# Kernel optimization log

Hardware: AMD Instinct MI355X
Metric: run time of the kernel (lower is better)

The kernel has to match this reference:

```python
import jax, jax.numpy as jnp
import numpy as np

N_STEPS = 7
N_TERMS = 4


def _sobel_kernel2d():
    dx = jnp.array([[-1.0, 0.0, 1.0], [-2.0, 0.0, 2.0], [-1.0, 0.0, 1.0]], dtype=jnp.float32)
    dy = jnp.array([[-1.0, -2.0, -1.0], [0.0, 0.0, 0.0], [1.0, 2.0, 1.0]], dtype=jnp.float32)
    return 0.125 * jnp.stack([dy, dx, dy, dx], 0)[:, None]  # [4,1,3,3]


def _grid_sample_bilinear(src, sx, sy):
    # src: [N,C,H,W]; sx,sy: [N,H,W] pixel coords (align_corners=False, zeros padding)
    N, C, H, W = src.shape
    x0 = jnp.floor(sx)
    y0 = jnp.floor(sy)
    wx = (sx - x0)[:, None]  # [N,1,H,W]
    wy = (sy - y0)[:, None]
    x0i = x0.astype(jnp.int32)
    y0i = y0.astype(jnp.int32)

    def gather(yi, xi):
        valid = ((xi >= 0) & (xi < W) & (yi >= 0) & (yi < H))
        xc = jnp.clip(xi, 0, W - 1)
        yc = jnp.clip(yi, 0, H - 1)
        v = jax.vmap(lambda im, y, x: im[:, y, x])(src, yc, xc)  # [N,C,H,W]
        return v * valid[:, None].astype(src.dtype)

    v00 = gather(y0i, x0i)
    v01 = gather(y0i, x0i + 1)
    v10 = gather(y0i + 1, x0i)
    v11 = gather(y0i + 1, x0i + 1)
    return (v00 * (1 - wx) * (1 - wy) + v01 * wx * (1 - wy)
            + v10 * (1 - wx) * wy + v11 * wx * wy)


def _transform(src, disp, gy, gx, H, W):
    # new pixel locations; torch normalizes with (size-1) but samples with
    # align_corners=False, net mapping: p -> p*S/(S-1) - 0.5
    py = gy + disp[:, 0]
    px = gx + disp[:, 1]
    sy = py * (H / (H - 1)) - 0.5
    sx = px * (W / (W - 1)) - 0.5
    return _grid_sample_bilinear(src, sx, sy)


def _jacobian2d(vel):
    # replicate-pad then depthwise sobel conv -> [N,2,2,H,W]
    N, _, H, W = vel.shape
    padded = jnp.pad(vel, ((0, 0), (0, 0), (1, 1), (1, 1)), mode='edge')
    jac = jax.lax.conv_general_dilated(
        padded, _sobel_kernel2d(), window_strides=(1, 1), padding='VALID',
        feature_group_count=2, dimension_numbers=('NCHW', 'OIHW', 'NCHW'))
    return jac.reshape(N, 2, 2, H, W)


def _logdet1p(jac, eps):
    # -sum_n (-eps)^n tr(J^n)/n over the 2x2 dims, per pixel -> [N,H,W]
    ld = jnp.zeros(jac.shape[:1] + jac.shape[-2:], dtype=jac.dtype)
    xn = jac
    for n in range(1, N_TERMS + 1):
        if n > 1:
            xn = jnp.einsum('nikhw,nkjhw->nijhw', xn, jac)
        tr = xn[:, 0, 0] + xn[:, 1, 1]
        ld = ld - ((-eps) ** n) * tr / n
    return ld


def _integrate(vel, logdet_jac):
    N, _, H, W = vel.shape
    gy, gx = jnp.meshgrid(jnp.arange(H, dtype=vel.dtype),
                          jnp.arange(W, dtype=vel.dtype), indexing='ij')
    eps = 2.0 ** (-N_STEPS)
    disp = eps * vel
    if logdet_jac:
        ldjac = _logdet1p(_jacobian2d(vel), eps)[:, None]  # [N,1,H,W]
    else:
        ldjac = None
    for _ in range(N_STEPS):
        disp = disp + _transform(disp, disp, gy, gx, H, W)
        if logdet_jac:
            ldjac = ldjac + _transform(ldjac, disp, gy, gx, H, W)
    return disp, ldjac


def setup_inputs() -> dict:
    key = jax.random.key(0)
    vel = jax.random.normal(key, (16, 2, 512, 512), dtype=jnp.float32)
    return {"vel": vel, "logdet_jac": 1}


def reference(vel, logdet_jac):
    return _integrate(vel, bool(logdet_jac))
```

## Files before the change

kernel.cpp:

```cpp
#include <hip/hip_runtime.h>


#define NB 16
#define HH 512
#define WW 512
#define HW (HH * WW)
#define TOT (NB * HW)
#define EPS 0.0078125f
#define DISP_ELEMS (NB * 2 * HW)
#define SC (512.0f / 511.0f)

typedef _Float16 f16;
typedef _Float16 f16x4 __attribute__((ext_vector_type(4)));

struct SampC {
    int yc0, xc0, yc1, xc1;
    float w00, w01, w10, w11;
};

__device__ __forceinline__ SampC make_sampc(float sy, float sx) {
    float fy = floorf(sy), fx = floorf(sx);
    float wy = sy - fy, wx = sx - fx;
    int y0 = (int)fy, x0 = (int)fx;
    int y1 = y0 + 1, x1 = x0 + 1;
    bool xv0 = (unsigned)x0 < (unsigned)WW;
    bool xv1 = (unsigned)x1 < (unsigned)WW;
    bool yv0 = (unsigned)y0 < (unsigned)HH;
    bool yv1 = (unsigned)y1 < (unsigned)HH;
    SampC s;
    s.xc0 = min(max(x0, 0), WW - 1); s.xc1 = min(max(x1, 0), WW - 1);
    s.yc0 = min(max(y0, 0), HH - 1); s.yc1 = min(max(y1, 0), HH - 1);
    float omwx = 1.0f - wx, omwy = 1.0f - wy;
    s.w00 = (xv0 && yv0) ? omwx * omwy : 0.0f;
    s.w01 = (xv1 && yv0) ? wx * omwy   : 0.0f;
    s.w10 = (xv0 && yv1) ? omwx * wy   : 0.0f;
    s.w11 = (xv1 && yv1) ? wx * wy     : 0.0f;
    return s;
}

__device__ __forceinline__ f16x4 step_rec(f16x4 rv, f16x4 g00, f16x4 g01,
                                          f16x4 g10, f16x4 g11, const SampC& s) {
    float d0 = (float)rv.x, d1 = (float)rv.y, l = (float)rv.z;
    float nd0 = d0 + s.w00 * (float)g00.x + s.w01 * (float)g01.x
                   + s.w10 * (float)g10.x + s.w11 * (float)g11.x;
    float nd1 = d1 + s.w00 * (float)g00.y + s.w01 * (float)g01.y
                   + s.w10 * (float)g10.y + s.w11 * (float)g11.y;
    float nl  = l  + s.w00 * (float)g00.z + s.w01 * (float)g01.z
                   + s.w10 * (float)g10.z + s.w11 * (float)g11.z;
    f16x4 w; w.x = (f16)nd0; w.y = (f16)nd1; w.z = (f16)nl; w.w = (f16)0.0f;
    return w;
}

__device__ __forceinline__ float rnd16(float v) { return (float)(f16)v; }

__device__ __forceinline__ void tile_map(int& img, int& ty0, int& tx0) {
    int bidx = blockIdx.x;
    int xcd = bidx & 7, sub = bidx >> 3;
    img = 2 * xcd + (sub >= 256 ? 1 : 0);
    int tile = sub & 255;
    tx0 = (tile & 15) << 5;
    ty0 = (tile >> 4) << 5;
}

__device__ __forceinline__ int remap_idx() {
    int bid = blockIdx.x;
    int task = ((bid & 7) << 11) | (bid >> 3);
    return task * 256 + threadIdx.x;
}

__global__ void __launch_bounds__(256) init_fused(const float* __restrict__ vel,
                                                  f16x4* __restrict__ rdst) {
    int idx = remap_idx();
    int n = idx >> 18;
    int rem = idx & (HW - 1);
    int y = rem >> 9, x = rem & (WW - 1);

    const float* v0 = vel + (size_t)n * 2 * HW;
    const float* v1 = v0 + HW;

    int ym = max(y - 1, 0), yp = min(y + 1, HH - 1);
    int xm = max(x - 1, 0), xp = min(x + 1, WW - 1);
    int r0 = ym * WW, r1 = y * WW, r2 = yp * WW;

    float A00 = v0[r0 + xm], A01 = v0[r0 + x], A02 = v0[r0 + xp];
    float A10 = v0[r1 + xm], A11 = v0[r1 + x], A12 = v0[r1 + xp];
    float A20 = v0[r2 + xm], A21 = v0[r2 + x], A22 = v0[r2 + xp];
    float B00 = v1[r0 + xm], B01 = v1[r0 + x], B02 = v1[r0 + xp];
    float B10 = v1[r1 + xm], B11 = v1[r1 + x], B12 = v1[r1 + xp];
    float B20 = v1[r2 + xm], B21 = v1[r2 + x], B22 = v1[r2 + xp];

    float a = 0.125f * ((A20 + 2.0f * A21 + A22) - (A00 + 2.0f * A01 + A02));
    float b = 0.125f * ((A02 + 2.0f * A12 + A22) - (A00 + 2.0f * A10 + A20));
    float c = 0.125f * ((B20 + 2.0f * B21 + B22) - (B00 + 2.0f * B01 + B02));
    float d = 0.125f * ((B02 + 2.0f * B12 + B22) - (B00 + 2.0f * B10 + B20));

    float xa = a, xb = b, xc = c, xd = d;
    float ld = EPS * (xa + xd);
    float na = xa * a + xb * c, nb = xa * b + xb * d;
    float nc = xc * a + xd * c, nd = xc * b + xd * d;
    xa = na; xb = nb; xc = nc; xd = nd;
    ld -= (EPS * EPS) * (xa + xd) * 0.5f;
    na = xa * a + xb * c; nb = xa * b + xb * d;
    nc = xc * a + xd * c; nd = xc * b + xd * d;
    xa = na; xb = nb; xc = nc; xd = nd;
    ld += (EPS * EPS * EPS) * (xa + xd) * (1.0f / 3.0f);
    na = xa * a + xb * c;
    nd = xc * b + xd * d;
    ld -= (EPS * EPS * EPS * EPS) * (na + nd) * 0.25f;

    float d0 = rnd16(EPS * A11);
    float d1 = rnd16(EPS * B11);

    float sy = fmaf((float)y + d0, SC, -0.5f);
    float sx = fmaf((float)x + d1, SC, -0.5f);
    SampC s = make_sampc(sy, sx);

    bool rlo = (sy < (float)y);
    bool clo = (sx < (float)x);

    float Ar0c0 = rlo ? A00 : A10, Ar0c1 = rlo ? A01 : A11, Ar0c2 = rlo ? A02 : A12;
    float Ar1c0 = rlo ? A10 : A20, Ar1c1 = rlo ? A11 : A21, Ar1c2 = rlo ? A12 : A22;
    float Br0c0 = rlo ? B00 : B10, Br0c1 = rlo ? B01 : B11, Br0c2 = rlo ? B02 : B12;
    float Br1c0 = rlo ? B10 : B20, Br1c1 = rlo ? B11 : B21, Br1c2 = rlo ? B12 : B22;

    float g00x = rnd16(EPS * (clo ? Ar0c0 : Ar0c1));
    float g01x = rnd16(EPS * (clo ? Ar0c1 : Ar0c2));
    float g10x = rnd16(EPS * (clo ? Ar1c0 : Ar1c1));
    float g11x = rnd16(EPS * (clo ? Ar1c1 : Ar1c2));
    float g00y = rnd16(EPS * (clo ? Br0c0 : Br0c1));
    float g01y = rnd16(EPS * (clo ? Br0c1 : Br0c2));
    float g10y = rnd16(EPS * (clo ? Br1c0 : Br1c1));
    float g11y = rnd16(EPS * (clo ? Br1c1 : Br1c2));

    float nd0 = d0 + s.w00 * g00x + s.w01 * g01x + s.w10 * g10x + s.w11 * g11x;
    float nd1 = d1 + s.w00 * g00y + s.w01 * g01y + s.w10 * g10y + s.w11 * g11y;

    f16x4 rec;
    rec.x = (f16)nd0; rec.y = (f16)nd1; rec.z = (f16)ld; rec.w = (f16)0.0f;
    rdst[(size_t)n * HW + rem] = rec;
}

template <int R1, int R2, int R3>
__global__ void __launch_bounds__(256, 4) step_triple(const f16x4* __restrict__ rsrc,
                                                      f16x4* __restrict__ rdst) {
    constexpr int M2d = 32 + 2 * R3;
    constexpr int M1d = 32 + 2 * (R2 + R3);
    constexpr int Ed  = 32 + 2 * (R1 + R2 + R3);
    __shared__ __align__(16) f16x4 IN[Ed][Ed + 1];
    __shared__ __align__(16) f16x4 M1[M1d][M1d + 1];
    f16x4 (*M2)[M2d + 1] = (f16x4 (*)[M2d + 1])&IN[0][0];

    int img, ty0, tx0;
    tile_map(img, ty0, tx0);
    int t = threadIdx.x;
    const f16x4* rp = rsrc + (size_t)img * HW;

    for (int i = t; i < Ed * Ed; i += 256) {
        int ey = i / Ed, ex = i - ey * Ed;
        int gy = min(max(ty0 - (R1 + R2 + R3) + ey, 0), HH - 1);
        int gx = min(max(tx0 - (R1 + R2 + R3) + ex, 0), WW - 1);
        IN[ey][ex] = rp[gy * WW + gx];
    }
    __syncthreads();

    {
        const int oy = ty0 - (R1 + R2 + R3), ox = tx0 - (R1 + R2 + R3);
        for (int i = t; i < M1d * M1d; i += 256) {
            int my = i / M1d, mx = i - my * M1d;
            int qy = ty0 - (R2 + R3) + my, qx = tx0 - (R2 + R3) + mx;
            f16x4 rv = IN[my + R1][mx + R1];
            float sy = fmaf((float)qy + (float)rv.x, SC, -0.5f);
            float sx = fmaf((float)qx + (float)rv.y, SC, -0.5f);
            SampC s = make_sampc(sy, sx);
            f16x4 g00 = IN[s.yc0 - oy][s.xc0 - ox];
            f16x4 g01 = IN[s.yc0 - oy][s.xc1 - ox];
            f16x4 g10 = IN[s.yc1 - oy][s.xc0 - ox];
            f16x4 g11 = IN[s.yc1 - oy][s.xc1 - ox];
            M1[my][mx] = step_rec(rv, g00, g01, g10, g11, s);
        }
    }
    __syncthreads();

    {
        const int oy = ty0 - (R2 + R3), ox = tx0 - (R2 + R3);
        for (int i = t; i < M2d * M2d; i += 256) {
            int my = i / M2d, mx = i - my * M2d;
            int qy = ty0 - R3 + my, qx = tx0 - R3 + mx;
            f16x4 rv = M1[my + R2][mx + R2];
            float sy = fmaf((float)qy + (float)rv.x, SC, -0.5f);
            float sx = fmaf((float)qx + (float)rv.y, SC, -0.5f);
            SampC s = make_sampc(sy, sx);
            f16x4 g00 = M1[s.yc0 - oy][s.xc0 - ox];
            f16x4 g01 = M1[s.yc0 - oy][s.xc1 - ox];
            f16x4 g10 = M1[s.yc1 - oy][s.xc0 - ox];
            f16x4 g11 = M1[s.yc1 - oy][s.xc1 - ox];
            M2[my][mx] = step_rec(rv, g00, g01, g10, g11, s);
        }
    }
    __syncthreads();

    {
        const int oy = ty0 - R3, ox = tx0 - R3;
        f16x4* wp = rdst + (size_t)img * HW;
        for (int i = t; i < 1024; i += 256) {
            int cy = i >> 5, cx = i & 31;
            int qy = ty0 + cy, qx = tx0 + cx;
            f16x4 rv = M2[cy + R3][cx + R3];
            float sy = fmaf((float)qy + (float)rv.x, SC, -0.5f);
            float sx = fmaf((float)qx + (float)rv.y, SC, -0.5f);
            SampC s = make_sampc(sy, sx);
            f16x4 g00 = M2[s.yc0 - oy][s.xc0 - ox];
            f16x4 g01 = M2[s.yc0 - oy][s.xc1 - ox];
            f16x4 g10 = M2[s.yc1 - oy][s.xc0 - ox];
            f16x4 g11 = M2[s.yc1 - oy][s.xc1 - ox];
            wp[qy * WW + qx] = step_rec(rv, g00, g01, g10, g11, s);
        }
    }
}

__global__ void __launch_bounds__(256) step_final(const f16x4* __restrict__ rsrc,
                                                  float* __restrict__ doutp,
                                                  float* __restrict__ loutp) {
    int idx = remap_idx();
    int n = idx >> 18;
    int rem = idx & (HW - 1);
    int y = rem >> 9, x = rem & (WW - 1);

    const f16x4* rp = rsrc + (size_t)n * HW;

    f16x4 rv = rp[rem];
    float d0 = (float)rv.x, d1 = (float)rv.y, l = (float)rv.z;

    float sy = fmaf((float)y + d0, SC, -0.5f);
    float sx = fmaf((float)x + d1, SC, -0.5f);
    SampC s = make_sampc(sy, sx);

    f16x4 g00 = rp[s.yc0 * WW + s.xc0], g01 = rp[s.yc0 * WW + s.xc1];
    f16x4 g10 = rp[s.yc1 * WW + s.xc0], g11 = rp[s.yc1 * WW + s.xc1];

    float nl = l + s.w00 * (float)g00.z + s.w01 * (float)g01.z
                 + s.w10 * (float)g10.z + s.w11 * (float)g11.z;

    float* pd = doutp + (size_t)n * 2 * HW;
    pd[rem]      = d0;
    pd[HW + rem] = d1;
    loutp[(size_t)n * HW + rem] = nl;
}

extern "C" void kernel_launch(void* const* d_in, const int* in_sizes, int n_in,
                              void* d_out, int out_size, void* d_ws, size_t ws_size,
                              hipStream_t stream) {
    const float* vel = (const float*)d_in[0];
    float* out = (float*)d_out;

    f16x4* rWS  = (f16x4*)d_ws;
    f16x4* rOUT = (f16x4*)d_out;

    dim3 block(256), gridT(4096), gridS(TOT / 256);

    init_fused<<<gridS, block, 0, stream>>>(vel, rWS);
    step_triple<2, 2, 2><<<gridT, block, 0, stream>>>(rWS, rOUT);
    step_triple<2, 3, 4><<<gridT, block, 0, stream>>>(rOUT, rWS);
    step_final<<<gridS, block, 0, stream>>>(rWS, out, out + DISP_ELEMS);
}
```

Before: 125.8 us.

## Split triple-step fused kernels into three two-step kernels with interior fast path

Replaces the two kernels that each fused three warp steps in shared memory with three kernels that each fuse two steps. This shrinks the halo and shared-memory footprint per tile at the cost of one extra global round trip. Interior tiles also get a specialised path that skips clamping and validity masking for both the halo load and the bilinear sampling. The fast path assumes displacements stay within the fixed radius bounds, which holds only if the per-step displacements are small.

After: 119.5 us. -5.0%, faster.

```diff
diff --git a/kernel.cpp b/kernel.cpp
--- a/kernel.cpp
+++ b/kernel.cpp
@@ -38,6 +38,18 @@
     return s;
 }
 
+__device__ __forceinline__ SampC make_sampc_fast(float sy, float sx) {
+    float fy = floorf(sy), fx = floorf(sx);
+    float wy = sy - fy, wx = sx - fx;
+    int y0 = (int)fy, x0 = (int)fx;
+    SampC s;
+    s.yc0 = y0; s.yc1 = y0 + 1; s.xc0 = x0; s.xc1 = x0 + 1;
+    float omwx = 1.0f - wx, omwy = 1.0f - wy;
+    s.w00 = omwx * omwy; s.w01 = wx * omwy;
+    s.w10 = omwx * wy;   s.w11 = wx * wy;
+    return s;
+}
+
 __device__ __forceinline__ f16x4 step_rec(f16x4 rv, f16x4 g00, f16x4 g01,
                                           f16x4 g10, f16x4 g11, const SampC& s) {
     float d0 = (float)rv.x, d1 = (float)rv.y, l = (float)rv.z;
@@ -140,79 +152,96 @@
     rdst[(size_t)n * HW + rem] = rec;
 }
 
-template <int R1, int R2, int R3>
-__global__ void __launch_bounds__(256, 4) step_triple(const f16x4* __restrict__ rsrc,
-                                                      f16x4* __restrict__ rdst) {
-    constexpr int M2d = 32 + 2 * R3;
-    constexpr int M1d = 32 + 2 * (R2 + R3);
-    constexpr int Ed  = 32 + 2 * (R1 + R2 + R3);
-    __shared__ __align__(16) f16x4 IN[Ed][Ed + 1];
-    __shared__ __align__(16) f16x4 M1[M1d][M1d + 1];
-    f16x4 (*M2)[M2d + 1] = (f16x4 (*)[M2d + 1])&IN[0][0];
+template <int R1, int R2>
+__global__ void __launch_bounds__(256, 4) step_pair(const f16x4* __restrict__ rsrc,
+                                                    f16x4* __restrict__ rdst) {
+    constexpr int MW = 32 + 2 * R2;
+    constexpr int EW = 32 + 2 * (R1 + R2);
+    __shared__ f16x4 IN[EW][EW + 1];
+    __shared__ f16x4 MID[MW][MW + 1];
 
     int img, ty0, tx0;
     tile_map(img, ty0, tx0);
     int t = threadIdx.x;
     const f16x4* rp = rsrc + (size_t)img * HW;
 
-    for (int i = t; i < Ed * Ed; i += 256) {
-        int ey = i / Ed, ex = i - ey * Ed;
-        int gy = min(max(ty0 - (R1 + R2 + R3) + ey, 0), HH - 1);
-        int gx = min(max(tx0 - (R1 + R2 + R3) + ex, 0), WW - 1);
-        IN[ey][ex] = rp[gy * WW + gx];
+    const int oyE = ty0 - (R1 + R2), oxE = tx0 - (R1 + R2);
+    const int oyM = ty0 - R2,        oxM = tx0 - R2;
+    bool safe = (tx0 >= 32) && (tx0 <= 448) && (ty0 >= 32) && (ty0 <= 448);
+
+    if (safe) {
+        for (int i = t; i < EW * EW; i += 256) {
+            int ey = i / EW, ex = i - ey * EW;
+            IN[ey][ex] = rp[(oyE + ey) * WW + (oxE + ex)];
+        }
+    } else {
+        for (int i = t; i < EW * EW; i += 256) {
+            int ey = i / EW, ex = i - ey * EW;
+            int gy = min(max(oyE + ey, 0), HH - 1);
+            int gx = min(max(oxE + ex, 0), WW - 1);
+            IN[ey][ex] = rp[gy * WW + gx];
+        }
     }
     __syncthreads();
 
-    {
-        const int oy = ty0 - (R1 + R2 + R3), ox = tx0 - (R1 + R2 + R3);
-        for (int i = t; i < M1d * M1d; i += 256) {
-            int my = i / M1d, mx = i - my * M1d;
-            int qy = ty0 - (R2 + R3) + my, qx = tx0 - (R2 + R3) + mx;
+    if (safe) {
+        for (int i = t; i < MW * MW; i += 256) {
+            int my = i / MW, mx = i - my * MW;
+            int qy = oyM + my, qx = oxM + mx;
             f16x4 rv = IN[my + R1][mx + R1];
             float sy = fmaf((float)qy + (float)rv.x, SC, -0.5f);
             float sx = fmaf((float)qx + (float)rv.y, SC, -0.5f);
+            SampC s = make_sampc_fast(sy, sx);
+            f16x4 g00 = IN[s.yc0 - oyE][s.xc0 - oxE];
+            f16x4 g01 = IN[s.yc0 - oyE][s.xc1 - oxE];
+            f16x4 g10 = IN[s.yc1 - oyE][s.xc0 - oxE];
+            f16x4 g11 = IN[s.yc1 - oyE][s.xc1 - oxE];
+            MID[my][mx] = step_rec(rv, g00, g01, g10, g11, s);
+        }
+    } else {
+        for (int i = t; i < MW * MW; i += 256) {
+            int my = i / MW, mx = i - my * MW;
+            int qy = oyM + my, qx = oxM + mx;
+            f16x4 rv = IN[my + R1][mx + R1];
+            float sy = fmaf((float)qy + (float)rv.x, SC, -0.5f);
+            float sx = fmaf((float)qx + (float)rv.y, SC, -0.5f);
             SampC s = make_sampc(sy, sx);
-            f16x4 g00 = IN[s.yc0 - oy][s.xc0 - ox];
-            f16x4 g01 = IN[s.yc0 - oy][s.xc1 - ox];
-            f16x4 g10 = IN[s.yc1 - oy][s.xc0 - ox];
-            f16x4 g11 = IN[s.yc1 - oy][s.xc1 - ox];
-            M1[my][mx] = step_rec(rv, g00, g01, g10, g11, s);
+            f16x4 g00 = IN[s.yc0 - oyE][s.xc0 - oxE];
+            f16x4 g01 = IN[s.yc0 - oyE][s.xc1 - oxE];
+            f16x4 g10 = IN[s.yc1 - oyE][s.xc0 - oxE];
+            f16x4 g11 = IN[s.yc1 - oyE][s.xc1 - oxE];
+            MID[my][mx] = step_rec(rv, g00, g01, g10, g11, s);
         }
     }
     __syncthreads();
 
-    {
-        const int oy = ty0 - (R2 + R3), ox = tx0 - (R2 + R3);
-        for (int i = t; i < M2d * M2d; i += 256) {
-            int my = i / M2d, mx = i - my * M2d;
-            int qy = ty0 - R3 + my, qx = tx0 - R3 + mx;
-            f16x4 rv = M1[my + R2][mx + R2];
-            float sy = fmaf((float)qy + (float)rv.x, SC, -0.5f);
-            float sx = fmaf((float)qx + (float)rv.y, SC, -0.5f);
-            SampC s = make_sampc(sy, sx);
-            f16x4 g00 = M1[s.yc0 - oy][s.xc0 - ox];
-            f16x4 g01 = M1[s.yc0 - oy][s.xc1 - ox];
-            f16x4 g10 = M1[s.yc1 - oy][s.xc0 - ox];
-            f16x4 g11 = M1[s.yc1 - oy][s.xc1 - ox];
-            M2[my][mx] = step_rec(rv, g00, g01, g10, g11, s);
-        }
-    }
-    __syncthreads();
-
-    {
-        const int oy = ty0 - R3, ox = tx0 - R3;
-        f16x4* wp = rdst + (size_t)img * HW;
+    f16x4* wp = rdst + (size_t)img * HW;
+    if (safe) {
         for (int i = t; i < 1024; i += 256) {
             int cy = i >> 5, cx = i & 31;
             int qy = ty0 + cy, qx = tx0 + cx;
-            f16x4 rv = M2[cy + R3][cx + R3];
+            f16x4 rv = MID[cy + R2][cx + R2];
+            float sy = fmaf((float)qy + (float)rv.x, SC, -0.5f);
+            float sx = fmaf((float)qx + (float)rv.y, SC, -0.5f);
+            SampC s = make_sampc_fast(sy, sx);
+            f16x4 g00 = MID[s.yc0 - oyM][s.xc0 - oxM];
+            f16x4 g01 = MID[s.yc0 - oyM][s.xc1 - oxM];
+            f16x4 g10 = MID[s.yc1 - oyM][s.xc0 - oxM];
+            f16x4 g11 = MID[s.yc1 - oyM][s.xc1 - oxM];
+            wp[qy * WW + qx] = step_rec(rv, g00, g01, g10, g11, s);
+        }
+    } else {
+        for (int i = t; i < 1024; i += 256) {
+            int cy = i >> 5, cx = i & 31;
+            int qy = ty0 + cy, qx = tx0 + cx;
+            f16x4 rv = MID[cy + R2][cx + R2];
             float sy = fmaf((float)qy + (float)rv.x, SC, -0.5f);
             float sx = fmaf((float)qx + (float)rv.y, SC, -0.5f);
             SampC s = make_sampc(sy, sx);
-            f16x4 g00 = M2[s.yc0 - oy][s.xc0 - ox];
-            f16x4 g01 = M2[s.yc0 - oy][s.xc1 - ox];
-            f16x4 g10 = M2[s.yc1 - oy][s.xc0 - ox];
-            f16x4 g11 = M2[s.yc1 - oy][s.xc1 - ox];
+            f16x4 g00 = MID[s.yc0 - oyM][s.xc0 - oxM];
+            f16x4 g01 = MID[s.yc0 - oyM][s.xc1 - oxM];
+            f16x4 g10 = MID[s.yc1 - oyM][s.xc0 - oxM];
+            f16x4 g11 = MID[s.yc1 - oyM][s.xc1 - oxM];
             wp[qy * WW + qx] = step_rec(rv, g00, g01, g10, g11, s);
         }
     }
@@ -253,13 +282,14 @@
     const float* vel = (const float*)d_in[0];
     float* out = (float*)d_out;
 
-    f16x4* rWS  = (f16x4*)d_ws;
-    f16x4* rOUT = (f16x4*)d_out;
+    f16x4* rA = (f16x4*)d_out;
+    f16x4* rB = (f16x4*)d_ws;
 
     dim3 block(256), gridT(4096), gridS(TOT / 256);
 
-    init_fused<<<gridS, block, 0, stream>>>(vel, rWS);
-    step_triple<2, 2, 2><<<gridT, block, 0, stream>>>(rWS, rOUT);
-    step_triple<2, 3, 4><<<gridT, block, 0, stream>>>(rOUT, rWS);
-    step_final<<<gridS, block, 0, stream>>>(rWS, out, out + DISP_ELEMS);
-}
+    init_fused<<<gridS, block, 0, stream>>>(vel, rA);
+    step_pair<2, 2><<<gridT, block, 0, stream>>>(rA, rB);
+    step_pair<2, 2><<<gridT, block, 0, stream>>>(rB, rA);
+    step_pair<3, 4><<<gridT, block, 0, stream>>>(rA, rB);
+    step_final<<<gridS, block, 0, stream>>>(rB, out, out + DISP_ELEMS);
+}
```
